# Kernel optimization log

Hardware: AMD Instinct MI355X
Metric: run time of the kernel (lower is better)

## Reference

```python
import jax, jax.numpy as jnp
import numpy as np

N = 50000      # nodes
E = 800000     # edges (avg degree 16)
F_IN = 256     # num_node_features
H = 256        # hidden_dim
L = 2          # num_message_passing_rounds - 1 hidden conv layers


def setup_inputs() -> dict:
    key = jax.random.key(0)
    ks = jax.random.split(key, 8)
    x = jax.random.normal(ks[0], (N, F_IN), dtype=jnp.float32)
    edge_index = jax.random.randint(ks[1], (2, E), 0, N, dtype=jnp.int32)
    init = lambda k, shape, fan: jax.random.normal(k, shape, dtype=jnp.float32) / np.float32(np.sqrt(fan))
    WA_in = init(ks[2], (F_IN, H), F_IN)   # proj_in.A weight (stored [in,out])
    WB_in = init(ks[3], (F_IN, H), F_IN)   # proj_in.B weight
    A_stack = init(ks[4], (L, H, H), H)    # conv layers' A weights
    B_stack = init(ks[5], (L, H, H), H)    # conv layers' B weights
    W_out = init(ks[6], (H, 1), H)         # proj_out weight
    b_out = jnp.zeros((1,), jnp.float32)   # proj_out bias
    return {"x": x, "edge_index": edge_index, "WA_in": WA_in, "WB_in": WB_in,
            "A_stack": A_stack, "B_stack": B_stack, "W_out": W_out, "b_out": b_out}


def reference(x, edge_index, WA_in, WB_in, A_stack, B_stack, W_out, b_out):
    src, dst = edge_index[0], edge_index[1]
    # in-degree per node; PyG scatter-mean divides by max(deg, 1)
    deg = jax.ops.segment_sum(jnp.ones((E,), x.dtype), dst, num_segments=N)
    inv_deg = (1.0 / jnp.maximum(deg, 1.0))[:, None]  # [N,1]

    def mean_agg(h):
        # gather x_j = h[src], scatter-mean into dst -> [N, d]
        return jax.ops.segment_sum(h[src], dst, num_segments=N) * inv_deg

    # proj_in: A(mean_msg) + B(x)
    h = mean_agg(x) @ WA_in + x @ WB_in
    # hidden conv rounds with sigmoid (use_relu=False)
    for i in range(L):
        h = jax.nn.sigmoid(mean_agg(h) @ A_stack[i] + h @ B_stack[i])
    # proj_out + squeeze (output_logits=True)
    return (h @ W_out + b_out).squeeze()  # [N]
```

## Files before the change

kernel.cpp:

```cpp
#include <hip/hip_runtime.h>

typedef unsigned short u16;
typedef unsigned int u32;
typedef __attribute__((ext_vector_type(8))) short short8;
typedef __attribute__((ext_vector_type(4))) float f32x4;
typedef __attribute__((ext_vector_type(2))) float f32x2;

__device__ __forceinline__ float bf2f(u16 u) {
    return __uint_as_float(((u32)u) << 16);
}
__device__ __forceinline__ u16 f2bf(float f) {
    u32 u = __float_as_uint(f);
    u += 0x7fff + ((u >> 16) & 1);
    return (u16)(u >> 16);
}
__device__ __forceinline__ u32 pack2(float a, float b) {
    return (u32)f2bf(a) | ((u32)f2bf(b) << 16);
}
__device__ __forceinline__ u32 pk_fp8x4(float f0, float f1, float f2, float f3) {
    int w = __builtin_amdgcn_cvt_pk_fp8_f32(f0, f1, 0, false);
    w = __builtin_amdgcn_cvt_pk_fp8_f32(f2, f3, w, true);
    return (u32)w;
}
__device__ __forceinline__ void acc4(float* a, u32 w) {
    f32x2 lo = __builtin_amdgcn_cvt_pk_f32_fp8((int)w, false);
    f32x2 hi = __builtin_amdgcn_cvt_pk_f32_fp8((int)w, true);
    a[0] += lo.x; a[1] += lo.y; a[2] += hi.x; a[3] += hi.y;
}
__device__ __forceinline__ void acc4m(float* a, u32 w, float m) {
    f32x2 lo = __builtin_amdgcn_cvt_pk_f32_fp8((int)w, false);
    f32x2 hi = __builtin_amdgcn_cvt_pk_f32_fp8((int)w, true);
    a[0] += m * lo.x; a[1] += m * lo.y; a[2] += m * hi.x; a[3] += m * hi.y;
}
__device__ __forceinline__ void acc16(float* a, uint4 v) {
    acc4(a + 0, v.x); acc4(a + 4, v.y); acc4(a + 8, v.z); acc4(a + 12, v.w);
}
__device__ __forceinline__ void acc16m(float* a, uint4 v, float m) {
    acc4m(a + 0, v.x, m); acc4m(a + 4, v.y, m); acc4m(a + 8, v.z, m); acc4m(a + 12, v.w, m);
}


__global__ void cvt_x_kernel(const float* __restrict__ x, u16* __restrict__ xb,
                             u32* __restrict__ xq, int n) {
    int i = blockIdx.x * 256 + threadIdx.x;
    int row = i >> 6;
    ushort4 o;
    u32 q;
    if (row < n) {
        float4 v = ((const float4*)x)[i];
        o.x = f2bf(v.x); o.y = f2bf(v.y); o.z = f2bf(v.z); o.w = f2bf(v.w);
        q = pk_fp8x4(v.x, v.y, v.z, v.w);
    } else {
        o.x = o.y = o.z = o.w = 0;
        q = 0;
    }
    ((ushort4*)xb)[i] = o;
    xq[i] = q;
}

__global__ void cvt_h_kernel(const u16* __restrict__ hb, uint2* __restrict__ hq, int ngroups) {
    int j = blockIdx.x * 256 + threadIdx.x;
    if (j >= ngroups) return;
    uint4 v = ((const uint4*)hb)[j];
    float f0 = bf2f(v.x & 0xffff), f1 = bf2f(v.x >> 16);
    float f2 = bf2f(v.y & 0xffff), f3 = bf2f(v.y >> 16);
    float f4 = bf2f(v.z & 0xffff), f5 = bf2f(v.z >> 16);
    float f6 = bf2f(v.w & 0xffff), f7 = bf2f(v.w >> 16);
    uint2 o;
    o.x = pk_fp8x4(f0, f1, f2, f3);
    o.y = pk_fp8x4(f4, f5, f6, f7);
    hq[j] = o;
}

__global__ void cvt_w_kernel(const float* __restrict__ WA, const float* __restrict__ WB,
                             const float* __restrict__ As, const float* __restrict__ Bs,
                             u16* __restrict__ wT, int nlayers) {
    int i = blockIdx.x * 256 + threadIdx.x;
    const int per = 256 * 512;
    if (i >= nlayers * per) return;
    int l = i / per;
    int rem = i - l * per;
    int nn = rem >> 9;
    int k = rem & 511;
    const float* Aw = (l == 0) ? WA : As + (size_t)(l - 1) * 65536;
    const float* Bw = (l == 0) ? WB : Bs + (size_t)(l - 1) * 65536;
    float v = (k < 256) ? Aw[(size_t)k * 256 + nn] : Bw[(size_t)(k - 256) * 256 + nn];
    wT[i] = f2bf(v);
}


__global__ __launch_bounds__(256) void hist_kernel(const int* __restrict__ dst,
                                                   int* __restrict__ ccnt, int e, int nb) {
    __shared__ int h[256];
    int tid = threadIdx.x;
    h[tid] = 0;
    __syncthreads();
    int e0 = blockIdx.x * 4096;
#pragma unroll
    for (int j = 0; j < 16; ++j) {
        int i = e0 + j * 256 + tid;
        if (i < e) atomicAdd(&h[dst[i] >> 8], 1);
    }
    __syncthreads();
    if (tid < nb) {
        int v = h[tid];
        if (v) atomicAdd(&ccnt[tid], v);
    }
}

__global__ __launch_bounds__(256) void scan_coarse_kernel(const int* __restrict__ ccnt,
                                                          int* __restrict__ cbase,
                                                          int* __restrict__ rowptr,
                                                          int nb, int n, int e) {
    __shared__ int sh[256];
    int t = threadIdx.x;
    int v = (t < nb) ? ccnt[t] : 0;
    int x = v;
    sh[t] = x; __syncthreads();
    for (int o = 1; o < 256; o <<= 1) {
        int y = (t >= o) ? sh[t - o] : 0;
        __syncthreads();
        x += y; sh[t] = x; __syncthreads();
    }
    if (t < nb) cbase[t] = x - v;
    if (t == 0) { cbase[nb] = e; rowptr[n] = e; }
}

__global__ __launch_bounds__(256) void passA_kernel(const int* __restrict__ src,
                                                    const int* __restrict__ dst,
                                                    const int* __restrict__ cbase,
                                                    int* __restrict__ cfill,
                                                    u32* __restrict__ tmp, int e, int nb) {
    __shared__ int ph[256], pb[256], pr[256], cb[256];
    __shared__ u32 ed[4096];
    int tid = threadIdx.x;
    ph[tid] = 0; pr[tid] = 0;
    cb[tid] = (tid < nb) ? cbase[tid] : 0;
    __syncthreads();
    int e0 = blockIdx.x * 4096;
#pragma unroll
    for (int j = 0; j < 16; ++j) {
        int i = e0 + j * 256 + tid;
        u32 p = 0xFFFFFFFFu;
        if (i < e) {
            int d = dst[i];
            p = ((u32)d << 16) | (u32)src[i];
            atomicAdd(&ph[d >> 8], 1);
        }
        ed[j * 256 + tid] = p;
    }
    __syncthreads();
    pb[tid] = (tid < nb && ph[tid]) ? atomicAdd(&cfill[tid], ph[tid]) : 0;
    __syncthreads();
#pragma unroll
    for (int j = 0; j < 16; ++j) {
        u32 p = ed[j * 256 + tid];
        if (p != 0xFFFFFFFFu) {
            int bk = p >> 24;
            int r = atomicAdd(&pr[bk], 1);
            tmp[cb[bk] + pb[bk] + r] = p;
        }
    }
}

__global__ __launch_bounds__(256) void passB_kernel(const u32* __restrict__ tmp,
                                                    const int* __restrict__ cbase,
                                                    int* __restrict__ rowptr,
                                                    float* __restrict__ invd,
                                                    int* __restrict__ srcs, int n) {
    __shared__ int h[256], loc[256], cnt2[256], sh[256];
    int b = blockIdx.x;
    int tid = threadIdx.x;
    int base = cbase[b];
    int cnt = cbase[b + 1] - base;
    int node0 = b << 8;
    h[tid] = 0; cnt2[tid] = 0;
    __syncthreads();
    for (int i = tid; i < cnt; i += 256)
        atomicAdd(&h[(tmp[base + i] >> 16) & 255], 1);
    __syncthreads();
    int c = h[tid];
    int x = c;
    sh[tid] = x; __syncthreads();
    for (int o = 1; o < 256; o <<= 1) {
        int y = (tid >= o) ? sh[tid - o] : 0;
        __syncthreads();
        x += y; sh[tid] = x; __syncthreads();
    }
    loc[tid] = x - c;
    int node = node0 + tid;
    if (node < n) {
        rowptr[node] = base + x - c;
        invd[node] = 1.0f / (float)(c > 0 ? c : 1);
    }
    __syncthreads();
    for (int i = tid; i < cnt; i += 256) {
        u32 p = tmp[base + i];
        int ln = (p >> 16) & 255;
        int r = atomicAdd(&cnt2[ln], 1);
        srcs[base + loc[ln] + r] = (int)(p & 0xffffu);
    }
}


__global__ __launch_bounds__(256) void agg_kernel(const unsigned char* __restrict__ q,
                                                  u16* __restrict__ mb,
                                                  const int* __restrict__ rowptr,
                                                  const int* __restrict__ srcs,
                                                  const float* __restrict__ invd,
                                                  int n, int npad) {
    int gw = (blockIdx.x * 256 + threadIdx.x) >> 6;
    int lane = threadIdx.x & 63;
    int qd = lane >> 4;
    int fl = lane & 15;
    if (gw >= npad) return;
    u16* orow = mb + (size_t)gw * 256;
    if (gw >= n) {
        if (lane < 16) {
            uint4 z; z.x = z.y = z.z = z.w = 0;
            uint4* p = (uint4*)(orow + lane * 16);
            p[0] = z; p[1] = z;
        }
        return;
    }
    int beg = rowptr[gw], end = rowptr[gw + 1];
    float a[16];
#pragma unroll
    for (int i = 0; i < 16; ++i) a[i] = 0.f;
    for (int base = beg; base < end; base += 64) {
        int cnt = end - base;
        if (cnt > 64) cnt = 64;
        int el = (lane < cnt) ? srcs[base + lane] : 0;
        int t = 0;
        for (; 4 * t + 8 <= cnt; t += 2) {
            int s0 = __shfl(el, 4 * t + qd);
            int s1 = __shfl(el, 4 * t + 4 + qd);
            uint4 v0 = *(const uint4*)(q + (size_t)s0 * 256 + fl * 16);
            uint4 v1 = *(const uint4*)(q + (size_t)s1 * 256 + fl * 16);
            acc16(a, v0);
            acc16(a, v1);
        }
        for (; 4 * t < cnt; ++t) {
            int ei = 4 * t + qd;
            int sj = __shfl(el, ei & 63);
            float m = (ei < cnt) ? 1.0f : 0.0f;
            uint4 v = *(const uint4*)(q + (size_t)sj * 256 + fl * 16);
            acc16m(a, v, m);
        }
    }
#pragma unroll
    for (int i = 0; i < 16; ++i) {
        a[i] += __shfl_xor(a[i], 16);
        a[i] += __shfl_xor(a[i], 32);
    }
    if (lane < 16) {
        float sc = invd[gw];
        uint4 o0, o1;
        o0.x = pack2(a[0] * sc, a[1] * sc);
        o0.y = pack2(a[2] * sc, a[3] * sc);
        o0.z = pack2(a[4] * sc, a[5] * sc);
        o0.w = pack2(a[6] * sc, a[7] * sc);
        o1.x = pack2(a[8] * sc, a[9] * sc);
        o1.y = pack2(a[10] * sc, a[11] * sc);
        o1.z = pack2(a[12] * sc, a[13] * sc);
        o1.w = pack2(a[14] * sc, a[15] * sc);
        uint4* p = (uint4*)(orow + lane * 16);
        p[0] = o0; p[1] = o1;
    }
}


__global__ __launch_bounds__(256, 2) void gemm_kernel(const u16* __restrict__ mA,
                                                      const u16* __restrict__ cur,
                                                      const u16* __restrict__ wT,
                                                      u16* __restrict__ outb,
                                                      const float* __restrict__ wo,
                                                      const float* __restrict__ bo,
                                                      float* __restrict__ out,
                                                      int n, int apply_sigmoid, int fin) {
    __shared__ u16 lA[128 * 32];
    __shared__ u16 lB[256 * 32];
    __shared__ float lO[2][128];
    int r0 = blockIdx.x * 128;
    int tid = threadIdx.x;
    int lane = tid & 63;
    int w = tid >> 6;
    int wrow = w >> 1, wcol = w & 1;
    int lrow = lane & 15, quad = lane >> 4;

    f32x4 acc[4][8] = {};

    for (int ks = 0; ks < 16; ++ks) {
        int k0 = ks * 32;
        const u16* srcA = (k0 < 256) ? mA : cur;
        int kk = k0 & 255;
        __syncthreads();
#pragma unroll
        for (int p = 0; p < 2; ++p) {
            int li = p * 256 + tid;
            int row = li >> 2;
            int seg = (li & 3) << 3;
            const u16* gA = srcA + (size_t)(r0 + row) * 256 + kk + seg;
            __builtin_amdgcn_global_load_lds(
                (__attribute__((address_space(1))) u32*)(gA),
                (__attribute__((address_space(3))) u32*)(lA + (size_t)li * 8), 16, 0, 0);
        }
#pragma unroll
        for (int p = 0; p < 4; ++p) {
            int li = p * 256 + tid;
            int row = li >> 2;
            int seg = (li & 3) << 3;
            const u16* gB = wT + (size_t)row * 512 + k0 + seg;
            __builtin_amdgcn_global_load_lds(
                (__attribute__((address_space(1))) u32*)(gB),
                (__attribute__((address_space(3))) u32*)(lB + (size_t)li * 8), 16, 0, 0);
        }
        __syncthreads();

        short8 a[4], b[8];
#pragma unroll
        for (int t = 0; t < 4; ++t)
            a[t] = *(const short8*)(lA + ((size_t)(wrow * 64 + t * 16 + lrow) * 32 + quad * 8));
#pragma unroll
        for (int t = 0; t < 8; ++t)
            b[t] = *(const short8*)(lB + ((size_t)(wcol * 128 + t * 16 + lrow) * 32 + quad * 8));
#pragma unroll
        for (int rt = 0; rt < 4; ++rt)
#pragma unroll
            for (int ct = 0; ct < 8; ++ct)
                acc[rt][ct] = __builtin_amdgcn_mfma_f32_16x16x32_bf16(a[rt], b[ct], acc[rt][ct], 0, 0, 0);
    }

    if (!fin) {
#pragma unroll
        for (int rt = 0; rt < 4; ++rt) {
            int rbase = r0 + wrow * 64 + rt * 16 + quad * 4;
#pragma unroll
            for (int r = 0; r < 4; ++r) {
                int row = rbase + r;
                if (row < n) {
#pragma unroll
                    for (int ct = 0; ct < 8; ++ct) {
                        float v = acc[rt][ct][r];
                        if (apply_sigmoid) v = 1.0f / (1.0f + __expf(-v));
                        outb[(size_t)row * 256 + wcol * 128 + ct * 16 + lrow] = f2bf(v);
                    }
                }
            }
        }
    } else {
        float wv[8];
#pragma unroll
        for (int ct = 0; ct < 8; ++ct) wv[ct] = wo[wcol * 128 + ct * 16 + lrow];
#pragma unroll
        for (int rt = 0; rt < 4; ++rt) {
#pragma unroll
            for (int r = 0; r < 4; ++r) {
                float s = 0.f;
#pragma unroll
                for (int ct = 0; ct < 8; ++ct) {
                    float v = acc[rt][ct][r];
                    v = 1.0f / (1.0f + __expf(-v));
                    s += v * wv[ct];
                }
                s += __shfl_xor(s, 1);
                s += __shfl_xor(s, 2);
                s += __shfl_xor(s, 4);
                s += __shfl_xor(s, 8);
                if (lrow == 0) {
                    int rowlocal = wrow * 64 + rt * 16 + quad * 4 + r;
                    lO[wcol][rowlocal] = s;
                }
            }
        }
        __syncthreads();
        if (tid < 128) {
            int row = r0 + tid;
            if (row < n) out[row] = lO[0][tid] + lO[1][tid] + bo[0];
        }
    }
}


extern "C" void kernel_launch(void* const* d_in, const int* in_sizes, int n_in,
                              void* d_out, int out_size, void* d_ws, size_t ws_size,
                              hipStream_t stream) {
    const float* x  = (const float*)d_in[0];
    const int*   ei = (const int*)d_in[1];
    const float* WA = (const float*)d_in[2];
    const float* WB = (const float*)d_in[3];
    const float* As = (const float*)d_in[4];
    const float* Bs = (const float*)d_in[5];
    const float* Wo = (const float*)d_in[6];
    const float* bo = (const float*)d_in[7];
    float* out = (float*)d_out;

    const int H = 256;
    int N = in_sizes[0] / H;
    int E = in_sizes[1] / 2;
    int L = in_sizes[4] / (H * H);
    int NPAD = (N + 127) & ~127;
    int NB = (N + 255) >> 8;

    char* wsp = (char*)d_ws;
    size_t off = 0;
    auto alloc = [&](size_t b) { size_t o = off; off += (b + 255) & ~(size_t)255; return o; };
    int*   rowptr = (int*)(wsp + alloc((size_t)(NPAD + 1) * 4));
    int*   ccnt   = (int*)(wsp + alloc(1024));
    int*   cbase  = (int*)(wsp + alloc(1032 + 256));
    int*   cfill  = (int*)(wsp + alloc(1024));
    float* invd   = (float*)(wsp + alloc((size_t)NPAD * 4));
    int*   srcs   = (int*)(wsp + alloc((size_t)E * 4));
    u16*   xb     = (u16*)(wsp + alloc((size_t)NPAD * H * 2));
    u16*   hbuf   = (u16*)(wsp + alloc((size_t)NPAD * H * 2));
    u16*   mb     = (u16*)(wsp + alloc((size_t)NPAD * H * 2));
    u32*   xq     = (u32*)(wsp + alloc((size_t)NPAD * H));
    uint2* hq     = (uint2*)(wsp + alloc((size_t)NPAD * H));
    u16*   wT     = (u16*)(wsp + alloc((size_t)(L + 1) * 512 * 256 * 2));
    u32*   tmp    = (u32*)mb;

    const int* esrc = ei;
    const int* edst = ei + E;

    hipMemsetAsync(ccnt, 0, 1024, stream);
    hipMemsetAsync(cfill, 0, 1024, stream);

    int gridE = (E + 4095) / 4096;
    cvt_x_kernel<<<NPAD / 4, 256, 0, stream>>>(x, xb, xq, N);
    cvt_w_kernel<<<((L + 1) * 512 * 256 + 255) / 256, 256, 0, stream>>>(WA, WB, As, Bs, wT, L + 1);
    hist_kernel<<<gridE, 256, 0, stream>>>(edst, ccnt, E, NB);
    scan_coarse_kernel<<<1, 256, 0, stream>>>(ccnt, cbase, rowptr, NB, N, E);
    passA_kernel<<<gridE, 256, 0, stream>>>(esrc, edst, cbase, cfill, tmp, E, NB);
    passB_kernel<<<NB, 256, 0, stream>>>(tmp, cbase, rowptr, invd, srcs, N);

    const u16* cur = xb;
    const unsigned char* curq = (const unsigned char*)xq;
    for (int s = 0; s <= L; ++s) {
        int fin = (s == L) ? 1 : 0;
        agg_kernel<<<NPAD / 4, 256, 0, stream>>>(curq, mb, rowptr, srcs, invd, N, NPAD);
        gemm_kernel<<<NPAD / 128, 256, 0, stream>>>(mb, cur, wT + (size_t)s * 512 * 256, hbuf,
                                                    Wo, bo, out, N, s > 0 ? 1 : 0, fin);
        if (!fin) {
            cvt_h_kernel<<<(N * 32 + 255) / 256, 256, 0, stream>>>(hbuf, hq, N * 32);
            cur = hbuf;
            curq = (const unsigned char*)hq;
        }
    }
}
```

Measured before the change: 341.8 us.

## Double-buffer GEMM LDS tiles, swizzle layout, shrink row tile to 64

Restructures the GEMM kernel to prefetch the next K-slice into a second LDS buffer while computing the current one, which removes one barrier per iteration. It also XOR-style rotates the 16-byte segments in LDS to reduce bank conflicts on the fragment reads. The row tile drops from 128 to 64, so each wave owns a 64-column strip and the grid doubles. The trade-off is less A/B reuse per block, since the weights are reloaded twice as often, and higher LDS use per block.

```diff
diff --git a/kernel.cpp b/kernel.cpp
--- a/kernel.cpp
+++ b/kernel.cpp
@@ -270,95 +270,104 @@
 }
 
 
-__global__ __launch_bounds__(256, 2) void gemm_kernel(const u16* __restrict__ mA,
-                                                      const u16* __restrict__ cur,
-                                                      const u16* __restrict__ wT,
-                                                      u16* __restrict__ outb,
-                                                      const float* __restrict__ wo,
-                                                      const float* __restrict__ bo,
-                                                      float* __restrict__ out,
-                                                      int n, int apply_sigmoid, int fin) {
-    __shared__ u16 lA[128 * 32];
-    __shared__ u16 lB[256 * 32];
-    __shared__ float lO[2][128];
-    int r0 = blockIdx.x * 128;
+__global__ __launch_bounds__(256) void gemm_kernel(const u16* __restrict__ mA,
+                                                   const u16* __restrict__ cur,
+                                                   const u16* __restrict__ wT,
+                                                   u16* __restrict__ outb,
+                                                   const float* __restrict__ wo,
+                                                   const float* __restrict__ bo,
+                                                   float* __restrict__ out,
+                                                   int n, int apply_sigmoid, int fin) {
+    __shared__ u16 lA[2][64 * 32];
+    __shared__ u16 lB[2][256 * 32];
+    __shared__ float lO[4][64];
+    int r0 = blockIdx.x * 64;
     int tid = threadIdx.x;
     int lane = tid & 63;
     int w = tid >> 6;
-    int wrow = w >> 1, wcol = w & 1;
     int lrow = lane & 15, quad = lane >> 4;
 
-    f32x4 acc[4][8] = {};
-
-    for (int ks = 0; ks < 16; ++ks) {
+    f32x4 acc[4][4] = {};
+
+    auto stage = [&](int ks, int b) {
         int k0 = ks * 32;
-        const u16* srcA = (k0 < 256) ? mA : cur;
+        const u16* sA = (k0 < 256) ? mA : cur;
         int kk = k0 & 255;
-        __syncthreads();
-#pragma unroll
-        for (int p = 0; p < 2; ++p) {
-            int li = p * 256 + tid;
+        {
+            int li = tid;
             int row = li >> 2;
-            int seg = (li & 3) << 3;
-            const u16* gA = srcA + (size_t)(r0 + row) * 256 + kk + seg;
+            int ls = ((li & 3) - row) & 3;
+            const u16* g = sA + (size_t)(r0 + row) * 256 + kk + ls * 8;
             __builtin_amdgcn_global_load_lds(
-                (__attribute__((address_space(1))) u32*)(gA),
-                (__attribute__((address_space(3))) u32*)(lA + (size_t)li * 8), 16, 0, 0);
+                (const __attribute__((address_space(1))) u32*)g,
+                (__attribute__((address_space(3))) u32*)(&lA[b][(size_t)li * 8]), 16, 0, 0);
         }
 #pragma unroll
         for (int p = 0; p < 4; ++p) {
             int li = p * 256 + tid;
             int row = li >> 2;
-            int seg = (li & 3) << 3;
-            const u16* gB = wT + (size_t)row * 512 + k0 + seg;
+            int ls = ((li & 3) - row) & 3;
+            const u16* g = wT + (size_t)row * 512 + k0 + ls * 8;
             __builtin_amdgcn_global_load_lds(
-                (__attribute__((address_space(1))) u32*)(gB),
-                (__attribute__((address_space(3))) u32*)(lB + (size_t)li * 8), 16, 0, 0);
-        }
+                (const __attribute__((address_space(1))) u32*)g,
+                (__attribute__((address_space(3))) u32*)(&lB[b][(size_t)li * 8]), 16, 0, 0);
+        }
+    };
+
+    stage(0, 0);
+    int buf = 0;
+    for (int ks = 0; ks < 16; ++ks) {
         __syncthreads();
-
-        short8 a[4], b[8];
-#pragma unroll
-        for (int t = 0; t < 4; ++t)
-            a[t] = *(const short8*)(lA + ((size_t)(wrow * 64 + t * 16 + lrow) * 32 + quad * 8));
-#pragma unroll
-        for (int t = 0; t < 8; ++t)
-            b[t] = *(const short8*)(lB + ((size_t)(wcol * 128 + t * 16 + lrow) * 32 + quad * 8));
+        if (ks < 15) stage(ks + 1, buf ^ 1);
+        short8 a[4], b4[4];
+#pragma unroll
+        for (int rt = 0; rt < 4; ++rt) {
+            int row = rt * 16 + lrow;
+            int ps = (quad + row) & 3;
+            a[rt] = *(const short8*)(&lA[buf][(size_t)row * 32 + ps * 8]);
+        }
+#pragma unroll
+        for (int ct = 0; ct < 4; ++ct) {
+            int row = w * 64 + ct * 16 + lrow;
+            int ps = (quad + row) & 3;
+            b4[ct] = *(const short8*)(&lB[buf][(size_t)row * 32 + ps * 8]);
+        }
 #pragma unroll
         for (int rt = 0; rt < 4; ++rt)
 #pragma unroll
-            for (int ct = 0; ct < 8; ++ct)
-                acc[rt][ct] = __builtin_amdgcn_mfma_f32_16x16x32_bf16(a[rt], b[ct], acc[rt][ct], 0, 0, 0);
+            for (int ct = 0; ct < 4; ++ct)
+                acc[rt][ct] = __builtin_amdgcn_mfma_f32_16x16x32_bf16(a[rt], b4[ct], acc[rt][ct], 0, 0, 0);
+        buf ^= 1;
     }
 
     if (!fin) {
 #pragma unroll
         for (int rt = 0; rt < 4; ++rt) {
-            int rbase = r0 + wrow * 64 + rt * 16 + quad * 4;
+            int rbase = r0 + rt * 16 + quad * 4;
 #pragma unroll
             for (int r = 0; r < 4; ++r) {
                 int row = rbase + r;
                 if (row < n) {
 #pragma unroll
-                    for (int ct = 0; ct < 8; ++ct) {
+                    for (int ct = 0; ct < 4; ++ct) {
                         float v = acc[rt][ct][r];
                         if (apply_sigmoid) v = 1.0f / (1.0f + __expf(-v));
-                        outb[(size_t)row * 256 + wcol * 128 + ct * 16 + lrow] = f2bf(v);
+                        outb[(size_t)row * 256 + w * 64 + ct * 16 + lrow] = f2bf(v);
                     }
                 }
             }
         }
     } else {
-        float wv[8];
-#pragma unroll
-        for (int ct = 0; ct < 8; ++ct) wv[ct] = wo[wcol * 128 + ct * 16 + lrow];
+        float wv[4];
+#pragma unroll
+        for (int ct = 0; ct < 4; ++ct) wv[ct] = wo[w * 64 + ct * 16 + lrow];
 #pragma unroll
         for (int rt = 0; rt < 4; ++rt) {
 #pragma unroll
             for (int r = 0; r < 4; ++r) {
                 float s = 0.f;
 #pragma unroll
-                for (int ct = 0; ct < 8; ++ct) {
+                for (int ct = 0; ct < 4; ++ct) {
                     float v = acc[rt][ct][r];
                     v = 1.0f / (1.0f + __expf(-v));
                     s += v * wv[ct];
@@ -367,16 +376,13 @@
                 s += __shfl_xor(s, 2);
                 s += __shfl_xor(s, 4);
                 s += __shfl_xor(s, 8);
-                if (lrow == 0) {
-                    int rowlocal = wrow * 64 + rt * 16 + quad * 4 + r;
-                    lO[wcol][rowlocal] = s;
-                }
+                if (lrow == 0) lO[w][rt * 16 + quad * 4 + r] = s;
             }
         }
         __syncthreads();
-        if (tid < 128) {
+        if (tid < 64) {
             int row = r0 + tid;
-            if (row < n) out[row] = lO[0][tid] + lO[1][tid] + bo[0];
+            if (row < n) out[row] = lO[0][tid] + lO[1][tid] + lO[2][tid] + lO[3][tid] + bo[0];
         }
     }
 }
@@ -438,8 +444,8 @@
     for (int s = 0; s <= L; ++s) {
         int fin = (s == L) ? 1 : 0;
         agg_kernel<<<NPAD / 4, 256, 0, stream>>>(curq, mb, rowptr, srcs, invd, N, NPAD);
-        gemm_kernel<<<NPAD / 128, 256, 0, stream>>>(mb, cur, wT + (size_t)s * 512 * 256, hbuf,
-                                                    Wo, bo, out, N, s > 0 ? 1 : 0, fin);
+        gemm_kernel<<<NPAD / 64, 256, 0, stream>>>(mb, cur, wT + (size_t)s * 512 * 256, hbuf,
+                                                   Wo, bo, out, N, s > 0 ? 1 : 0, fin);
         if (!fin) {
             cvt_h_kernel<<<(N * 32 + 255) / 256, 256, 0, stream>>>(hbuf, hq, N * 32);
             cur = hbuf;
```

Measured after the change: 365.0 us. 6.8% more time.
